# Performance work log

Measured on AMD Instinct MI355X. Metric: run time of the kernel, lower is better.

The kernel has to match this reference:

```python
import jax, jax.numpy as jnp
import numpy as np

USER = 100000
ITEM = 100000
LATDIM = 64
ETYPE = 8
GNN_LAYERS = 2
HYPER_NUM = 128
N_EDGES = 100000


def setup_inputs() -> dict:
    key = jax.random.key(0)
    ks = jax.random.split(key, 7)
    # xavier-ish scaled params
    uEmbeds = jax.random.normal(ks[0], (USER, LATDIM), dtype=jnp.float32) * 0.05
    iEmbeds = jax.random.normal(ks[1], (ITEM, LATDIM), dtype=jnp.float32) * 0.05
    edgeTrans = jax.random.normal(ks[2], (ETYPE, LATDIM, LATDIM), dtype=jnp.float32) * 0.1
    src = jax.random.randint(ks[3], (N_EDGES,), 0, USER, dtype=jnp.int64 if jax.config.jax_enable_x64 else jnp.int32)
    tgt = jax.random.randint(ks[4], (N_EDGES,), 0, ITEM, dtype=src.dtype)
    val = jax.random.randint(ks[5], (N_EDGES,), 0, ETYPE, dtype=src.dtype)
    hyper = jax.random.normal(ks[6], (N_EDGES, HYPER_NUM), dtype=jnp.float32)
    return {"uEmbeds": uEmbeds, "iEmbeds": iEmbeds, "edgeTrans": edgeTrans,
            "hyper": hyper, "src": src, "tgt": tgt, "val": val}


def _hgnn_layer(edgeEmbeds, hyper):
    act = lambda x: jax.nn.leaky_relu(x, 0.5)
    # [d, H] = embeds^T @ hyper
    hyperEmbeds = act(jnp.einsum('ed,eh->dh', edgeEmbeds, hyper))
    # [E, d] = (hyperEmbeds @ hyper^T)^T
    nodeEmbeds = act(jnp.einsum('eh,dh->ed', hyper, hyperEmbeds))
    return nodeEmbeds


def reference(uEmbeds, iEmbeds, edgeTrans, hyper, src, tgt, val):
    srcE = uEmbeds[src]                       # [E, d] gather
    trans = edgeTrans[val]                    # [E, d, d] gather (large)
    # per-edge row-vector x matrix, then elementwise mult with tgt embeds
    edgeEmbeds = jnp.einsum('ed,edk->ek', srcE, trans) * iEmbeds[tgt]  # [E, d]
    for _ in range(GNN_LAYERS):
        edgeEmbeds = _hgnn_layer(edgeEmbeds, hyper) + edgeEmbeds
    srcOut = jax.ops.segment_sum(edgeEmbeds, src, num_segments=USER)  # sparse.sum over dim 1
    tgtOut = jax.ops.segment_sum(edgeEmbeds, tgt, num_segments=ITEM)  # sparse.sum over dim 0
    return (srcOut, tgtOut)
```

## Files before the change

kernel.cpp:

```cpp
#include <hip/hip_runtime.h>

#define E_N     100000
#define USER_N  100000
#define NROW    200000
#define NB_ACC  256
#define BIN_CAP 16384
#define E_PAD   114688
#define ACC_NCH 7
#define ACC_CHUNK 64
#define BUCKET_CAP 16
#define NB_INIT 782

typedef __bf16 bf16x8 __attribute__((ext_vector_type(8)));
typedef __bf16 bf16x4 __attribute__((ext_vector_type(4)));
typedef float  f32x4  __attribute__((ext_vector_type(4)));

__device__ __forceinline__ float leaky(float x) { return x > 0.f ? x : 0.5f * x; }

__global__ void initKernel(int* __restrict__ cnt, int* __restrict__ cnt8) {
  const int i = blockIdx.x * 256 + threadIdx.x;
  if (i < NROW + 2) cnt[i] = 0;
  if (i < 8) cnt8[i] = 0;
}

__global__ void binKernel(const int* __restrict__ val, const int* __restrict__ src,
                          const int* __restrict__ tgt,
                          int* __restrict__ perm, int* __restrict__ permSrc,
                          int* __restrict__ permTgt,
                          int* __restrict__ cnt8, int* __restrict__ cnt,
                          int* __restrict__ list) {
  __shared__ int lh[8], lbase[8];
  const int tid = threadIdx.x;
  if (tid < 8) lh[tid] = 0;
  __syncthreads();
  const int e = blockIdx.x * 256 + tid;
  int v = -1, slot = 0, s = 0, t = 0;
  if (e < E_N) {
    v = val[e]; s = src[e]; t = tgt[e];
    slot = atomicAdd(&lh[v], 1);
    const int ps = atomicAdd(&cnt[s], 1);
    if (ps < BUCKET_CAP) list[(size_t)s * BUCKET_CAP + ps] = e;
    const int pt = atomicAdd(&cnt[USER_N + t], 1);
    if (pt < BUCKET_CAP) list[(size_t)(USER_N + t) * BUCKET_CAP + pt] = e;
  }
  __syncthreads();
  if (tid < 8) lbase[tid] = atomicAdd(&cnt8[tid], lh[tid]);
  __syncthreads();
  if (v >= 0) {
    const int p = v * BIN_CAP + lbase[v] + slot;
    perm[p] = e; permSrc[p] = s; permTgt[p] = t;
  }
}

__global__ void __launch_bounds__(256) convertHyperTKernel(const float* __restrict__ hyper,
                                                           __bf16* __restrict__ hyperT,
                                                           __bf16* __restrict__ hyperB) {
  __shared__ __bf16 sT[128][72];
  const int tid = threadIdx.x;
  const int e0 = blockIdx.x * 64;
  const int h = tid >> 1, eoff = (tid & 1) * 32;
  if (e0 >= E_N) {
    const float4 z = make_float4(0.f, 0.f, 0.f, 0.f);
    #pragma unroll
    for (int q = 0; q < 4; ++q)
      *(float4*)((char*)(hyperT + (size_t)h * E_PAD + e0 + eoff) + q * 16) = z;
    return;
  }
  #pragma unroll
  for (int r = 0; r < 8; ++r) {
    const int idx = r * 256 + tid;
    const int e = idx >> 5, h4 = (idx & 31) * 4;
    float4 v = make_float4(0.f, 0.f, 0.f, 0.f);
    if (e0 + e < E_N) {
      v = *(const float4*)(hyper + (size_t)(e0 + e) * 128 + h4);
      bf16x4 pk;
      pk[0] = (__bf16)v.x; pk[1] = (__bf16)v.y; pk[2] = (__bf16)v.z; pk[3] = (__bf16)v.w;
      *(bf16x4*)(hyperB + (size_t)(e0 + e) * 128 + h4) = pk;
    }
    sT[h4 + 0][e] = (__bf16)v.x; sT[h4 + 1][e] = (__bf16)v.y;
    sT[h4 + 2][e] = (__bf16)v.z; sT[h4 + 3][e] = (__bf16)v.w;
  }
  __syncthreads();
  #pragma unroll
  for (int q = 0; q < 8; ++q) {
    const bf16x4 v = *(const bf16x4*)&sT[h][eoff + q * 4];
    *(bf16x4*)(hyperT + (size_t)h * E_PAD + e0 + eoff + q * 4) = v;
  }
}

__global__ void __launch_bounds__(256) stageAGemmKernel(
    const float* __restrict__ uE, const float* __restrict__ iE, const float* __restrict__ T,
    const int* __restrict__ permSrc, const int* __restrict__ permTgt,
    const int* __restrict__ perm, const int* __restrict__ cnt8,
    float* __restrict__ edge) {
  __shared__ float sT[64 * 68];
  __shared__ float sA[64 * 68];
  __shared__ int sIdxS[64], sIdxT[64];
  const int v  = blockIdx.y;
  const int nE = min(cnt8[v], BIN_CAP);
  const int t0 = blockIdx.x * 64;
  if (t0 >= nE) return;
  const int tid = threadIdx.x;
  if (tid < 64)  sIdxS[tid] = (t0 + tid < nE) ? permSrc[v * BIN_CAP + t0 + tid] : 0;
  else if (tid < 128) {
    const int l = tid - 64;
    sIdxT[l] = (t0 + l < nE) ? permTgt[v * BIN_CAP + t0 + l] : 0;
  }
  __syncthreads();
  #pragma unroll
  for (int r = 0; r < 4; ++r) {
    const int idx = r * 256 + tid;
    const int d = idx >> 4, kq = (idx & 15) * 4;
    *(float4*)&sT[d * 68 + kq] = *(const float4*)(T + (size_t)v * 4096 + d * 64 + kq);
  }
  #pragma unroll
  for (int r = 0; r < 4; ++r) {
    const int idx = r * 256 + tid;
    const int e = idx >> 4, dq = (idx & 15) * 4;
    float4 x = make_float4(0.f, 0.f, 0.f, 0.f);
    if (t0 + e < nE) x = *(const float4*)(uE + (size_t)sIdxS[e] * 64 + dq);
    *(float4*)&sA[e * 68 + dq] = x;
  }
  __syncthreads();
  const int e0 = (tid >> 4) * 4;
  const int k0 = (tid & 15) * 4;
  float acc[4][4];
  #pragma unroll
  for (int j = 0; j < 4; ++j)
    #pragma unroll
    for (int k = 0; k < 4; ++k) acc[j][k] = 0.f;
  #pragma unroll 4
  for (int db = 0; db < 16; ++db) {
    float4 a4[4], t4[4];
    #pragma unroll
    for (int j = 0; j < 4; ++j) a4[j] = *(const float4*)&sA[(e0 + j) * 68 + db * 4];
    #pragma unroll
    for (int q = 0; q < 4; ++q) t4[q] = *(const float4*)&sT[(db * 4 + q) * 68 + k0];
    #pragma unroll
    for (int j = 0; j < 4; ++j) {
      const float aj[4] = {a4[j].x, a4[j].y, a4[j].z, a4[j].w};
      #pragma unroll
      for (int q = 0; q < 4; ++q) {
        const float a = aj[q];
        acc[j][0] += a * t4[q].x;
        acc[j][1] += a * t4[q].y;
        acc[j][2] += a * t4[q].z;
        acc[j][3] += a * t4[q].w;
      }
    }
  }
  #pragma unroll
  for (int j = 0; j < 4; ++j) {
    const int et = t0 + e0 + j;
    if (et < nE) {
      const int eIdx = perm[v * BIN_CAP + et];
      const int tj = sIdxT[e0 + j];
      const float4 iv = *(const float4*)(iE + (size_t)tj * 64 + k0);
      float4 r;
      r.x = acc[j][0] * iv.x; r.y = acc[j][1] * iv.y;
      r.z = acc[j][2] * iv.z; r.w = acc[j][3] * iv.w;
      *(float4*)(edge + (size_t)eIdx * 64 + k0) = r;
    }
  }
}

__global__ void __launch_bounds__(512) hyperAccumMfmaKernel(
    const float* __restrict__ edge, const __bf16* __restrict__ hyperT,
    float* __restrict__ partials) {
  __shared__ __bf16 sE[2][64][72];
  const int tid  = threadIdx.x;
  const int lane = tid & 63;
  const int wave = tid >> 6;
  const int l16 = lane & 15, quad = lane >> 4;
  const int e0base = blockIdx.x * (ACC_NCH * ACC_CHUNK);
  const int d  = tid & 63;
  const int eg = tid >> 6;

  float rv[8];
  auto gload = [&](int c) {
    const int ebase = e0base + c * ACC_CHUNK + eg * 8;
    const float* p = edge + (size_t)ebase * 64 + d;
    if (ebase + 8 <= E_N) {
      #pragma unroll
      for (int i = 0; i < 8; ++i) rv[i] = p[i * 64];
    } else {
      #pragma unroll
      for (int i = 0; i < 8; ++i) rv[i] = (ebase + i < E_N) ? p[i * 64] : 0.f;
    }
  };
  auto swrite = [&](int b) {
    bf16x8 pk;
    #pragma unroll
    for (int i = 0; i < 8; ++i) pk[i] = (__bf16)rv[i];
    *(bf16x8*)&sE[b][d][eg * 8] = pk;
  };

  f32x4 acc[4];
  #pragma unroll
  for (int dt = 0; dt < 4; ++dt) acc[dt] = (f32x4){0.f, 0.f, 0.f, 0.f};

  gload(0); swrite(0);
  __syncthreads();
  for (int c = 0; c < ACC_NCH; ++c) {
    const int nb = c & 1;
    if (c + 1 < ACC_NCH) gload(c + 1);
    #pragma unroll
    for (int ks = 0; ks < 2; ++ks) {
      const int eoff = c * ACC_CHUNK + ks * 32 + quad * 8;
      const bf16x8 B = *(const bf16x8*)(hyperT + (size_t)(wave * 16 + l16) * E_PAD + e0base + eoff);
      bf16x8 A[4];
      #pragma unroll
      for (int dt = 0; dt < 4; ++dt)
        A[dt] = *(const bf16x8*)&sE[nb][dt * 16 + l16][ks * 32 + quad * 8];
      #pragma unroll
      for (int dt = 0; dt < 4; ++dt)
        acc[dt] = __builtin_amdgcn_mfma_f32_16x16x32_bf16(A[dt], B, acc[dt], 0, 0, 0);
    }
    if (c + 1 < ACC_NCH) {
      __syncthreads();
      swrite(nb ^ 1);
      __syncthreads();
    }
  }
  float* pp = partials + (size_t)blockIdx.x * 8192;
  const int h = wave * 16 + l16;
  #pragma unroll
  for (int dt = 0; dt < 4; ++dt)
    #pragma unroll
    for (int reg = 0; reg < 4; ++reg) {
      const int dd = dt * 16 + quad * 4 + reg;
      pp[dd * 128 + h] = acc[dt][reg];
    }
}

__global__ void __launch_bounds__(256) reduceKernel(const float* __restrict__ partials,
                                                    __bf16* __restrict__ HEtT) {
  __shared__ float sd[8][33];
  const int tid = threadIdx.x;
  const int o = blockIdx.x * 32 + (tid & 31);
  const int g = tid >> 5;
  float s = 0.f;
  #pragma unroll 4
  for (int b = g * 32; b < (g + 1) * 32; ++b) s += partials[(size_t)b * 8192 + o];
  sd[g][tid & 31] = s;
  __syncthreads();
  if (tid < 32) {
    float t = 0.f;
    #pragma unroll
    for (int k = 0; k < 8; ++k) t += sd[k][tid];
    HEtT[blockIdx.x * 32 + tid] = (__bf16)leaky(t);
  }
}

__global__ void __launch_bounds__(256) nodeUpdateMfmaKernel(
    const __bf16* __restrict__ HEtT, const __bf16* __restrict__ hyperB,
    float* __restrict__ edge) {
  const int tid  = threadIdx.x;
  const int lane = tid & 63;
  const int wave = tid >> 6;
  const int l16 = lane & 15, quad = lane >> 4;
  bf16x8 Bf[4][4];
  #pragma unroll
  for (int kc = 0; kc < 4; ++kc)
    #pragma unroll
    for (int dt = 0; dt < 4; ++dt)
      Bf[kc][dt] = *(const bf16x8*)(HEtT + (dt * 16 + l16) * 128 + kc * 32 + quad * 8);
  const int wv = blockIdx.x * 4 + wave;
  for (int t = wv; t < E_N / 16; t += 2048) {
    const int e0 = t * 16;
    bf16x8 A[4];
    #pragma unroll
    for (int kc = 0; kc < 4; ++kc)
      A[kc] = *(const bf16x8*)(hyperB + (size_t)(e0 + l16) * 128 + kc * 32 + quad * 8);
    f32x4 acc[4];
    #pragma unroll
    for (int dt = 0; dt < 4; ++dt) acc[dt] = (f32x4){0.f, 0.f, 0.f, 0.f};
    #pragma unroll
    for (int kc = 0; kc < 4; ++kc)
      #pragma unroll
      for (int dt = 0; dt < 4; ++dt)
        acc[dt] = __builtin_amdgcn_mfma_f32_16x16x32_bf16(A[kc], Bf[kc][dt], acc[dt], 0, 0, 0);
    #pragma unroll
    for (int dt = 0; dt < 4; ++dt) {
      const int d = dt * 16 + l16;
      #pragma unroll
      for (int reg = 0; reg < 4; ++reg) {
        const int e = e0 + quad * 4 + reg;
        float* ep = edge + (size_t)e * 64 + d;
        *ep = *ep + leaky(acc[dt][reg]);
      }
    }
  }
}

__global__ void gatherSumKernel(const float* __restrict__ edge,
                                const int* __restrict__ cnt,
                                const int* __restrict__ list,
                                float* __restrict__ out) {
  const int tid = threadIdx.x;
  const int sub = tid & 15;
  const int grpInWave = (tid >> 4) & 3;
  const int gid = blockIdx.x * 16 + (tid >> 4);
  const int nG = gridDim.x * 16;
  for (int r = gid; r < NROW; r += nG) {
    const int n = min(cnt[r], BUCKET_CAP);
    int eL = (sub < n) ? list[(size_t)r * BUCKET_CAP + sub] : 0;
    float4 acc = make_float4(0.f, 0.f, 0.f, 0.f);
    for (int i = 0; i < n; ++i) {
      const int e = __shfl(eL, grpInWave * 16 + i, 64);
      const float4 v = *(const float4*)(edge + (size_t)e * 64 + sub * 4);
      acc.x += v.x; acc.y += v.y; acc.z += v.z; acc.w += v.w;
    }
    *(float4*)(out + (size_t)r * 64 + sub * 4) = acc;
  }
}

extern "C" void kernel_launch(void* const* d_in, const int* in_sizes, int n_in,
                              void* d_out, int out_size, void* d_ws, size_t ws_size,
                              hipStream_t stream) {
  const float* uE    = (const float*)d_in[0];
  const float* iE    = (const float*)d_in[1];
  const float* T     = (const float*)d_in[2];
  const float* hyper = (const float*)d_in[3];
  const int*   src   = (const int*)d_in[4];
  const int*   tgt   = (const int*)d_in[5];
  const int*   val   = (const int*)d_in[6];
  float* out = (float*)d_out;
  float* ws  = (float*)d_ws;

  float*  edge     = ws;
  float*  partials = ws + 6400000;
  __bf16* HEtT     = (__bf16*)(ws + 6400000 + 4194304 + 65536);
  int* perm    = (int*)partials;
  int* permSrc = perm + 8 * BIN_CAP;
  int* permTgt = permSrc + 8 * BIN_CAP;
  int* cnt8    = permTgt + 8 * BIN_CAP;
  int* cnt  = (int*)(ws + 6400000 + 4194304 + 65536 + 4096);
  int* list = cnt + (NROW + 4);
  __bf16* hyperT = (__bf16*)(ws + 15136256);
  __bf16* hyperB = (__bf16*)(ws + 22476288);

  initKernel<<<NB_INIT, 256, 0, stream>>>(cnt, cnt8);
  binKernel<<<(E_N + 255) / 256, 256, 0, stream>>>(val, src, tgt, perm, permSrc, permTgt, cnt8, cnt, list);
  convertHyperTKernel<<<E_PAD / 64, 256, 0, stream>>>(hyper, hyperT, hyperB);
  stageAGemmKernel<<<dim3(BIN_CAP / 64, 8), 256, 0, stream>>>(uE, iE, T, permSrc, permTgt, perm, cnt8, edge);

  for (int layer = 0; layer < 2; ++layer) {
    hyperAccumMfmaKernel<<<NB_ACC, 512, 0, stream>>>(edge, hyperT, partials);
    reduceKernel<<<256, 256, 0, stream>>>(partials, HEtT);
    nodeUpdateMfmaKernel<<<512, 256, 0, stream>>>(HEtT, hyperB, edge);
  }

  gatherSumKernel<<<6250, 256, 0, stream>>>(edge, cnt, list, out);
}
```

Measured before the change: 287.8 us.

## Compute per-edge transform with bf16 MFMA instead of FP32 LDS GEMM

Replaces the FP32 shared-memory register-tiled GEMM in stage A with a wave-level bf16 MFMA 16x16x32 kernel. Each wave handles 16 edges, loads uEmbeds rows directly into registers as bf16, and reads a pre-transposed bf16 copy of edgeTrans. That copy is produced inside initKernel. The change removes the LDS staging and the FP32 FMA loop. In exchange it lowers input precision to bf16 and makes the output stores and iEmbeds loads scalar rather than float4.

```diff
diff --git a/kernel.cpp b/kernel.cpp
--- a/kernel.cpp
+++ b/kernel.cpp
@@ -17,10 +17,20 @@
 
 __device__ __forceinline__ float leaky(float x) { return x > 0.f ? x : 0.5f * x; }
 
-__global__ void initKernel(int* __restrict__ cnt, int* __restrict__ cnt8) {
-  const int i = blockIdx.x * 256 + threadIdx.x;
+__global__ void initKernel(int* __restrict__ cnt, int* __restrict__ cnt8,
+                           const float* __restrict__ T, __bf16* __restrict__ Tt) {
+  const int b = blockIdx.x;
+  const int i = b * 256 + threadIdx.x;
   if (i < NROW + 2) cnt[i] = 0;
   if (i < 8) cnt8[i] = 0;
+  if (b < 8) {
+    const float* Tv = T + (size_t)b * 4096;
+    __bf16* Tb = Tt + (size_t)b * 4096;
+    for (int idx = threadIdx.x; idx < 4096; idx += 256) {
+      const int d = idx >> 6, k = idx & 63;
+      Tb[k * 64 + d] = (__bf16)Tv[idx];
+    }
+  }
 }
 
 __global__ void binKernel(const int* __restrict__ val, const int* __restrict__ src,
@@ -88,78 +98,67 @@
   }
 }
 
-__global__ void __launch_bounds__(256) stageAGemmKernel(
-    const float* __restrict__ uE, const float* __restrict__ iE, const float* __restrict__ T,
+__global__ void __launch_bounds__(256) stageAMfmaKernel(
+    const float* __restrict__ uE, const float* __restrict__ iE, const __bf16* __restrict__ Tt,
     const int* __restrict__ permSrc, const int* __restrict__ permTgt,
     const int* __restrict__ perm, const int* __restrict__ cnt8,
     float* __restrict__ edge) {
-  __shared__ float sT[64 * 68];
-  __shared__ float sA[64 * 68];
-  __shared__ int sIdxS[64], sIdxT[64];
   const int v  = blockIdx.y;
   const int nE = min(cnt8[v], BIN_CAP);
-  const int t0 = blockIdx.x * 64;
+  if (blockIdx.x * 64 >= nE) return;
+  const int tid  = threadIdx.x;
+  const int lane = tid & 63;
+  const int wave = tid >> 6;
+  const int l16 = lane & 15, quad = lane >> 4;
+  const int t0 = blockIdx.x * 64 + wave * 16;
   if (t0 >= nE) return;
-  const int tid = threadIdx.x;
-  if (tid < 64)  sIdxS[tid] = (t0 + tid < nE) ? permSrc[v * BIN_CAP + t0 + tid] : 0;
-  else if (tid < 128) {
-    const int l = tid - 64;
-    sIdxT[l] = (t0 + l < nE) ? permTgt[v * BIN_CAP + t0 + l] : 0;
-  }
-  __syncthreads();
-  #pragma unroll
-  for (int r = 0; r < 4; ++r) {
-    const int idx = r * 256 + tid;
-    const int d = idx >> 4, kq = (idx & 15) * 4;
-    *(float4*)&sT[d * 68 + kq] = *(const float4*)(T + (size_t)v * 4096 + d * 64 + kq);
-  }
-  #pragma unroll
-  for (int r = 0; r < 4; ++r) {
-    const int idx = r * 256 + tid;
-    const int e = idx >> 4, dq = (idx & 15) * 4;
-    float4 x = make_float4(0.f, 0.f, 0.f, 0.f);
-    if (t0 + e < nE) x = *(const float4*)(uE + (size_t)sIdxS[e] * 64 + dq);
-    *(float4*)&sA[e * 68 + dq] = x;
-  }
-  __syncthreads();
-  const int e0 = (tid >> 4) * 4;
-  const int k0 = (tid & 15) * 4;
-  float acc[4][4];
-  #pragma unroll
-  for (int j = 0; j < 4; ++j)
-    #pragma unroll
-    for (int k = 0; k < 4; ++k) acc[j][k] = 0.f;
-  #pragma unroll 4
-  for (int db = 0; db < 16; ++db) {
-    float4 a4[4], t4[4];
-    #pragma unroll
-    for (int j = 0; j < 4; ++j) a4[j] = *(const float4*)&sA[(e0 + j) * 68 + db * 4];
-    #pragma unroll
-    for (int q = 0; q < 4; ++q) t4[q] = *(const float4*)&sT[(db * 4 + q) * 68 + k0];
-    #pragma unroll
-    for (int j = 0; j < 4; ++j) {
-      const float aj[4] = {a4[j].x, a4[j].y, a4[j].z, a4[j].w};
-      #pragma unroll
-      for (int q = 0; q < 4; ++q) {
-        const float a = aj[q];
-        acc[j][0] += a * t4[q].x;
-        acc[j][1] += a * t4[q].y;
-        acc[j][2] += a * t4[q].z;
-        acc[j][3] += a * t4[q].w;
+
+  bf16x8 Bf[2][4];
+  #pragma unroll
+  for (int kc = 0; kc < 2; ++kc)
+    #pragma unroll
+    for (int nt = 0; nt < 4; ++nt)
+      Bf[kc][nt] = *(const bf16x8*)(Tt + (size_t)v * 4096 + (nt * 16 + l16) * 64 + kc * 32 + quad * 8);
+
+  const int pbase = v * BIN_CAP + t0;
+  const bool liveRow = (t0 + l16 < nE);
+  const int sIdx = liveRow ? permSrc[pbase + l16] : 0;
+  const int tIdx = liveRow ? permTgt[pbase + l16] : 0;
+  const int eIdx = liveRow ? perm[pbase + l16]    : 0;
+
+  bf16x8 A[2];
+  #pragma unroll
+  for (int kc = 0; kc < 2; ++kc) {
+    const float* ap = uE + (size_t)sIdx * 64 + kc * 32 + quad * 8;
+    const float4 f0 = *(const float4*)ap;
+    const float4 f1 = *(const float4*)(ap + 4);
+    bf16x8 a;
+    a[0] = (__bf16)f0.x; a[1] = (__bf16)f0.y; a[2] = (__bf16)f0.z; a[3] = (__bf16)f0.w;
+    a[4] = (__bf16)f1.x; a[5] = (__bf16)f1.y; a[6] = (__bf16)f1.z; a[7] = (__bf16)f1.w;
+    A[kc] = a;
+  }
+
+  f32x4 acc[4];
+  #pragma unroll
+  for (int nt = 0; nt < 4; ++nt) acc[nt] = (f32x4){0.f, 0.f, 0.f, 0.f};
+  #pragma unroll
+  for (int kc = 0; kc < 2; ++kc)
+    #pragma unroll
+    for (int nt = 0; nt < 4; ++nt)
+      acc[nt] = __builtin_amdgcn_mfma_f32_16x16x32_bf16(A[kc], Bf[kc][nt], acc[nt], 0, 0, 0);
+
+  const int qb = lane & 48;
+  #pragma unroll
+  for (int reg = 0; reg < 4; ++reg) {
+    const int j  = quad * 4 + reg;
+    const int tj = __shfl(tIdx, qb | j, 64);
+    const int gj = __shfl(eIdx, qb | j, 64);
+    if (t0 + j < nE) {
+      #pragma unroll
+      for (int nt = 0; nt < 4; ++nt) {
+        const int k = nt * 16 + l16;
+        edge[(size_t)gj * 64 + k] = acc[nt][reg] * iE[(size_t)tj * 64 + k];
       }
-    }
-  }
-  #pragma unroll
-  for (int j = 0; j < 4; ++j) {
-    const int et = t0 + e0 + j;
-    if (et < nE) {
-      const int eIdx = perm[v * BIN_CAP + et];
-      const int tj = sIdxT[e0 + j];
-      const float4 iv = *(const float4*)(iE + (size_t)tj * 64 + k0);
-      float4 r;
-      r.x = acc[j][0] * iv.x; r.y = acc[j][1] * iv.y;
-      r.z = acc[j][2] * iv.z; r.w = acc[j][3] * iv.w;
-      *(float4*)(edge + (size_t)eIdx * 64 + k0) = r;
     }
   }
 }
@@ -339,11 +338,12 @@
   int* list = cnt + (NROW + 4);
   __bf16* hyperT = (__bf16*)(ws + 15136256);
   __bf16* hyperB = (__bf16*)(ws + 22476288);
-
-  initKernel<<<NB_INIT, 256, 0, stream>>>(cnt, cnt8);
+  __bf16* Tt     = (__bf16*)(ws + 28876288);
+
+  initKernel<<<NB_INIT, 256, 0, stream>>>(cnt, cnt8, T, Tt);
   binKernel<<<(E_N + 255) / 256, 256, 0, stream>>>(val, src, tgt, perm, permSrc, permTgt, cnt8, cnt, list);
   convertHyperTKernel<<<E_PAD / 64, 256, 0, stream>>>(hyper, hyperT, hyperB);
-  stageAGemmKernel<<<dim3(BIN_CAP / 64, 8), 256, 0, stream>>>(uE, iE, T, permSrc, permTgt, perm, cnt8, edge);
+  stageAMfmaKernel<<<dim3(BIN_CAP / 64, 8), 256, 0, stream>>>(uE, iE, Tt, permSrc, permTgt, perm, cnt8, edge);
 
   for (int layer = 0; layer < 2; ++layer) {
     hyperAccumMfmaKernel<<<NB_ACC, 512, 0, stream>>>(edge, hyperT, partials);
```

New measurement: 285.1 us. About the same (-1.0%).
